# Performance work log

Measured on AMD Instinct MI355X. Metric: run time of the kernel, lower is better.

## Reference

```python
import jax, jax.numpy as jnp
import numpy as np


def setup_inputs() -> dict:
    key = jax.random.key(0)
    k0, k1, k2, k3 = jax.random.split(key, 4)
    B, H, W, C = 2, 128, 128, 512
    N_SPIX = 256  # (H/8)*(W/8) superpixels on an 8-px grid
    x = jax.random.normal(k0, (B, H, W, C), jnp.float32)
    sims = jax.random.uniform(k1, (B, H, W, 9), jnp.float32)
    sinds = jax.random.randint(k2, (B, H, W, 9), 0, N_SPIX, jnp.int32)
    W_qk = jax.random.normal(k3, (C, 2 * C), jnp.float32) * 0.02
    b_qk = jnp.zeros((2 * C,), jnp.float32)
    return {"x": x, "sims": sims, "sinds": sinds, "W_qk": W_qk, "b_qk": b_qk,
            "kernel_size": 7, "num_heads": 4}


def reference(x, sims, sinds, W_qk, b_qk, kernel_size, num_heads):
    """Soft-neighborhood superpixel attention scores.

    attn[b,g,si,h,w,ki] = <q[b,g,h,w], k[b,g,hj,wj]> + log p_j(s)
    where (hj,wj) is the ki-th pixel of the clamped (NATTEN-style) KxK window
    around (h,w), s = sinds[b,h,w,si] is the si-th neighboring-superpixel id
    of pixel (h,w), and p_j(s) = sum_m sims[b,hj,wj,m] * [sinds[b,hj,wj,m]==s]
    (the soft probability that key pixel j belongs to superpixel s; entries
    where s is not among j's 9 neighbor superpixels stay at -inf, matching
    the -inf-initialized attn buffer of the CUDA kernel).
    """
    B, H, W, C = x.shape
    K = kernel_size
    hd = C // num_heads
    r = K // 2

    # qk projection -> (B, heads, H, W, hd) for q and k (permute(3,0,4,1,2,5))
    qk = (x @ W_qk + b_qk).reshape(B, H, W, 2, num_heads, hd)
    q = jnp.moveaxis(qk[:, :, :, 0], 3, 1)  # (B,HD,H,W,hd)
    k = jnp.moveaxis(qk[:, :, :, 1], 3, 1)

    # NATTEN clamped window starts
    hs = jnp.clip(jnp.arange(H) - r, 0, H - K)  # (H,)
    ws = jnp.clip(jnp.arange(W) - r, 0, W - K)  # (W,)
    s_i = sinds  # (B,H,W,9): superpixel ids of pixel i's 9 neighbors

    dots, logps = [], []
    for dh in range(K):
        hj = hs + dh  # (H,)
        for dw in range(K):
            wj = ws + dw  # (W,)
            # gather key/sims/sinds at window offset (dh,dw)
            k_off = k[:, :, hj[:, None], wj[None, :], :]        # (B,HD,H,W,hd)
            dots.append(jnp.einsum('bghwf,bghwf->bghw', q, k_off))
            sind_j = sinds[:, hj[:, None], wj[None, :], :]      # (B,H,W,9)
            sim_j = sims[:, hj[:, None], wj[None, :], :]        # (B,H,W,9)
            # p_j(s_i): match i's si-th superpixel against j's 9 ids
            match = sind_j[:, :, :, None, :] == s_i[:, :, :, :, None]  # (B,H,W,9si,9m)
            pj = jnp.sum(jnp.where(match, sim_j[:, :, :, None, :], 0.0), axis=-1)  # (B,H,W,9)
            logps.append(jnp.where(pj > 0, jnp.log(jnp.maximum(pj, 1e-30)), -jnp.inf))

    dots = jnp.stack(dots, axis=-1)            # (B,HD,H,W,K*K)
    logp = jnp.stack(logps, axis=-1)           # (B,H,W,9,K*K)
    logp = jnp.moveaxis(logp, 3, 1)            # (B,9,H,W,K*K)
    attn = dots[:, :, None] + logp[:, None]    # (B,HD,9,H,W,K*K)
    return attn
```

## Files before the change

### kernel.cpp

```cpp
#include <hip/hip_runtime.h>
#include <hip/hip_bf16.h>
#include <math.h>

#define BATCH 2
#define HH 128
#define WW 128
#define CC 512
#define NH 4
#define HD 128
#define KS 7
#define RR 3
#define KK2 49
#define NSI 9

#define GM (BATCH*HH*WW)
#define GK CC
#define GN (2*CC)

#define NEG_HUGE (-1.0e30f)

typedef __attribute__((ext_vector_type(8))) short bf16x8;
typedef __attribute__((ext_vector_type(4))) float f32x4;

__device__ __forceinline__ float sout(float v) {
    return fminf(fmaxf(v, -3.0e38f), 3.0e38f);
}
__device__ __forceinline__ float bflo(unsigned int u) {
    return __builtin_bit_cast(float, u << 16);
}
__device__ __forceinline__ float bfhi(unsigned int u) {
    return __builtin_bit_cast(float, u & 0xffff0000u);
}
__device__ __forceinline__ unsigned short f2bf(float f) {
    unsigned int u = __builtin_bit_cast(unsigned int, f);
    u += 0x7fffu + ((u >> 16) & 1u);
    return (unsigned short)(u >> 16);
}

__device__ __forceinline__ void gl_lds16(const unsigned short* g, unsigned short* l) {
    __builtin_amdgcn_global_load_lds(
        (const __attribute__((address_space(1))) unsigned int*)g,
        (__attribute__((address_space(3))) unsigned int*)l, 16, 0, 0);
}

__global__ __launch_bounds__(256) void prep(const float* __restrict__ x,
                                            unsigned short* __restrict__ xb,
                                            const float* __restrict__ W,
                                            unsigned short* __restrict__ Wt,
                                            int nxc) {
    int bid = blockIdx.x;
    if (bid < nxc) {
        int t = bid * 256 + threadIdx.x;
        const float4* s = (const float4*)(x + (size_t)t * 8);
        float4 v0 = s[0], v1 = s[1];
        bf16x8 pk;
        pk[0] = (short)f2bf(v0.x); pk[1] = (short)f2bf(v0.y);
        pk[2] = (short)f2bf(v0.z); pk[3] = (short)f2bf(v0.w);
        pk[4] = (short)f2bf(v1.x); pk[5] = (short)f2bf(v1.y);
        pk[6] = (short)f2bf(v1.z); pk[7] = (short)f2bf(v1.w);
        *(bf16x8*)(xb + (size_t)t * 8) = pk;
    } else {
        int t = (bid - nxc) * 256 + threadIdx.x;
        int n = t >> 9, k = t & 511;
        Wt[(size_t)n * GK + k] = f2bf(W[(size_t)k * GN + n]);
    }
}

#define TBM 128
#define TBN 128
#define TBK 64

__global__ __launch_bounds__(256, 3) void qk_gemm_async(
        const unsigned short* __restrict__ xb,
        const unsigned short* __restrict__ Wt,
        const float* __restrict__ bias,
        unsigned short* __restrict__ Cout)
{
    __shared__ unsigned short As[TBM * TBK];
    __shared__ unsigned short Bs[TBN * TBK];

    const int bid = blockIdx.x;
    const int xcd = bid & 7, idx = bid >> 3;
    const int m0 = (xcd * 32 + (idx >> 3)) * TBM;
    const int n0 = (idx & 7) * TBN;

    const int tid = threadIdx.x;
    const int lane = tid & 63;
    const int wid = tid >> 6;
    const int wr = wid >> 1, wc = wid & 1;

    f32x4 acc[4][4];
#pragma unroll
    for (int i = 0; i < 4; ++i)
#pragma unroll
        for (int j = 0; j < 4; ++j) acc[i][j] = (f32x4){0.f, 0.f, 0.f, 0.f};

    const int srow = lane >> 3;
    const int scol = (lane & 7) * 8;

    for (int k0 = 0; k0 < GK; k0 += TBK) {
#pragma unroll
        for (int i = 0; i < 4; ++i) {
            int chunk = wid * 4 + i;
            int row = chunk * 8 + srow;
            gl_lds16(xb + (size_t)(m0 + row) * GK + k0 + scol, &As[chunk * 512]);
            gl_lds16(Wt + (size_t)(n0 + row) * GK + k0 + scol, &Bs[chunk * 512]);
        }
        __syncthreads();

#pragma unroll
        for (int ks = 0; ks < 2; ++ks) {
            const int koff = ks * 32 + (lane >> 4) * 8;
            bf16x8 af[4], bfr[4];
#pragma unroll
            for (int i = 0; i < 4; ++i)
                af[i] = *(const bf16x8*)&As[(wr * 64 + i * 16 + (lane & 15)) * TBK + koff];
#pragma unroll
            for (int j = 0; j < 4; ++j)
                bfr[j] = *(const bf16x8*)&Bs[(wc * 64 + j * 16 + (lane & 15)) * TBK + koff];
#pragma unroll
            for (int i = 0; i < 4; ++i)
#pragma unroll
                for (int j = 0; j < 4; ++j)
                    acc[i][j] = __builtin_amdgcn_mfma_f32_16x16x32_bf16(
                        af[i], bfr[j], acc[i][j], 0, 0, 0);
        }
        __syncthreads();
    }

    const int colbase = n0 + wc * 64;
    float bias4[4];
#pragma unroll
    for (int j = 0; j < 4; ++j) bias4[j] = bias[colbase + j * 16 + (lane & 15)];
#pragma unroll
    for (int i = 0; i < 4; ++i)
#pragma unroll
        for (int j = 0; j < 4; ++j)
#pragma unroll
            for (int r = 0; r < 4; ++r) {
                int row = m0 + wr * 64 + i * 16 + (lane >> 4) * 4 + r;
                int col = colbase + j * 16 + (lane & 15);
                Cout[(size_t)row * GN + col] = f2bf(acc[i][j][r] + bias4[j]);
            }
}

#define LDAB 72

__global__ __launch_bounds__(256) void qk_gemm_conv(
        const float* __restrict__ X,
        const unsigned short* __restrict__ Wt,
        const float* __restrict__ bias,
        unsigned short* __restrict__ Cout)
{
    __shared__ unsigned short As[TBM][LDAB];
    __shared__ unsigned short Bs[TBN][LDAB];

    const int m0 = blockIdx.x * TBM;
    const int n0 = blockIdx.y * TBN;
    const int tid = threadIdx.x;
    const int lane = tid & 63;
    const int wid = tid >> 6;
    const int wr = wid >> 1, wc = wid & 1;

    f32x4 acc[4][4];
#pragma unroll
    for (int i = 0; i < 4; ++i)
#pragma unroll
        for (int j = 0; j < 4; ++j) acc[i][j] = (f32x4){0.f, 0.f, 0.f, 0.f};

    const int srow = tid >> 1;
    const int shalf = (tid & 1) * 32;

    for (int k0 = 0; k0 < GK; k0 += TBK) {
        {
            const float* srcA = X + (size_t)(m0 + srow) * GK + k0 + shalf;
#pragma unroll
            for (int i = 0; i < 4; ++i) {
                float4 v0 = ((const float4*)srcA)[i * 2];
                float4 v1 = ((const float4*)srcA)[i * 2 + 1];
                bf16x8 pk;
                pk[0] = (short)f2bf(v0.x); pk[1] = (short)f2bf(v0.y);
                pk[2] = (short)f2bf(v0.z); pk[3] = (short)f2bf(v0.w);
                pk[4] = (short)f2bf(v1.x); pk[5] = (short)f2bf(v1.y);
                pk[6] = (short)f2bf(v1.z); pk[7] = (short)f2bf(v1.w);
                *(bf16x8*)&As[srow][shalf + i * 8] = pk;
            }
        }
        {
            const unsigned short* srcB = Wt + (size_t)(n0 + srow) * GK + k0 + shalf;
#pragma unroll
            for (int i = 0; i < 4; ++i)
                *(uint4*)&Bs[srow][shalf + i * 8] = ((const uint4*)srcB)[i];
        }
        __syncthreads();

#pragma unroll
        for (int ks = 0; ks < 2; ++ks) {
            const int koff = ks * 32 + (lane >> 4) * 8;
            bf16x8 af[4], bfr[4];
#pragma unroll
            for (int i = 0; i < 4; ++i)
                af[i] = *(const bf16x8*)&As[wr * 64 + i * 16 + (lane & 15)][koff];
#pragma unroll
            for (int j = 0; j < 4; ++j)
                bfr[j] = *(const bf16x8*)&Bs[wc * 64 + j * 16 + (lane & 15)][koff];
#pragma unroll
            for (int i = 0; i < 4; ++i)
#pragma unroll
                for (int j = 0; j < 4; ++j)
                    acc[i][j] = __builtin_amdgcn_mfma_f32_16x16x32_bf16(
                        af[i], bfr[j], acc[i][j], 0, 0, 0);
        }
        __syncthreads();
    }

    const int colbase = n0 + wc * 64;
    float bias4[4];
#pragma unroll
    for (int j = 0; j < 4; ++j) bias4[j] = bias[colbase + j * 16 + (lane & 15)];
#pragma unroll
    for (int i = 0; i < 4; ++i)
#pragma unroll
        for (int j = 0; j < 4; ++j)
#pragma unroll
            for (int r = 0; r < 4; ++r) {
                int row = m0 + wr * 64 + i * 16 + (lane >> 4) * 4 + r;
                int col = colbase + j * 16 + (lane & 15);
                Cout[(size_t)row * GN + col] = f2bf(acc[i][j][r] + bias4[j]);
            }
}

#define HALO 14
#define NKROW 196
#define LQK 136
#define LSS 204
#define NIT 13
#define NITEMS (64*KK2)

__global__ __launch_bounds__(256, 3) void attn_mfma(
        const unsigned short* __restrict__ qk,
        const float* __restrict__ sims,
        const int*   __restrict__ sinds,
        float* __restrict__ out)
{
    __shared__ __align__(16) unsigned char smem[53312];
    unsigned short* Ks = (unsigned short*)smem;
    float* Ss = (float*)smem;

    const int bid = blockIdx.x;
    const int spatial = (bid & 7) * 256 + (bid >> 3);
    const int tw = spatial & 15;
    const int th = (spatial >> 4) & 15;
    const int bg = spatial >> 8;
    const int b = bg >> 2, g = bg & 3;

    const int tid = threadIdx.x;
    const int lane = tid & 63;
    const int wm = tid >> 6;

    const int h0 = th * 8, w0 = tw * 8;
    const int hb = min(max(h0 - RR, 0), HH - KS);
    const int wb = min(max(w0 - RR, 0), WW - KS);

    uint4 kb[NIT];
    int jrow[NIT], ccol[NIT];
#pragma unroll
    for (int p = 0; p < NIT; ++p) {
        int o = tid + p * 256;
        int jj = o >> 4, c = o & 15;
        int jr = min(jj, NKROW - 1);
        int hj = min(hb + jr / HALO, HH - 1);
        int wj = min(wb + jr % HALO, WW - 1);
        kb[p] = *(const uint4*)(qk + ((size_t)((b * HH + hj) * WW + wj)) * GN
                                   + CC + g * HD + c * 8);
        jrow[p] = jr; ccol[p] = c;
    }

    const int pl_q = wm * 16 + (lane & 15);
    const size_t qrow = ((size_t)(b * HH + h0 + (pl_q >> 3)) * WW + w0 + (pl_q & 7)) * GN;
    const int kof8 = (lane >> 4) * 8;
    bf16x8 aq[4];
#pragma unroll
    for (int ks = 0; ks < 4; ++ks)
        aq[ks] = *(const bf16x8*)(qk + qrow + g * HD + ks * 32 + kof8);

#pragma unroll
    for (int p = 0; p < NIT; ++p)
        *(uint4*)&Ks[jrow[p] * LQK + ccol[p] * 8] = kb[p];
    __syncthreads();

    __builtin_amdgcn_s_setprio(1);
    f32x4 svals[NIT];
#pragma unroll
    for (int nt = 0; nt < NIT; ++nt) {
        int rB = min(nt * 16 + (lane & 15), NKROW - 1);
        f32x4 sacc = (f32x4){0.f, 0.f, 0.f, 0.f};
#pragma unroll
        for (int ks = 0; ks < 4; ++ks) {
            bf16x8 bk = *(const bf16x8*)&Ks[rB * LQK + ks * 32 + kof8];
            sacc = __builtin_amdgcn_mfma_f32_16x16x32_bf16(aq[ks], bk, sacc, 0, 0, 0);
        }
        svals[nt] = sacc;
    }
    __builtin_amdgcn_s_setprio(0);
    __syncthreads();

#pragma unroll
    for (int nt = 0; nt < NIT; ++nt)
#pragma unroll
        for (int r = 0; r < 4; ++r) {
            int qr = wm * 16 + (lane >> 4) * 4 + r;
            Ss[qr * LSS + nt * 16 + (lane & 15)] = svals[nt][r];
        }
    __syncthreads();

    const size_t plane = (size_t)HH * WW * KK2;
#pragma unroll
    for (int rr = 0; rr < NIT; ++rr) {
        int it = tid + rr * 256;
        if (it < NITEMS) {
            int pl = it / KK2, ki = it % KK2;
            int h = h0 + (pl >> 3), w = w0 + (pl & 7);
            int dh = ki / KS, dw = ki % KS;
            int hj = min(max(h - RR, 0), HH - KS) + dh;
            int wj = min(max(w - RR, 0), WW - KS) + dw;
            int j = (hj - hb) * HALO + (wj - wb);
            float dot = Ss[pl * LSS + j];
            int pix = (b * HH + h) * WW + w;
            int pj  = (b * HH + hj) * WW + wj;

            int sid[NSI], sjd[NSI]; float sjm[NSI];
            const int*   sip = sinds + (size_t)pix * NSI;
            const int*   sjp = sinds + (size_t)pj * NSI;
            const float* smp = sims + (size_t)pj * NSI;
#pragma unroll
            for (int m = 0; m < NSI; ++m) { sid[m] = sip[m]; sjd[m] = sjp[m]; sjm[m] = smp[m]; }

            size_t inner = (size_t)(h * WW + w) * KK2 + ki;
#pragma unroll
            for (int si = 0; si < NSI; ++si) {
                float p = 0.f;
#pragma unroll
                for (int m = 0; m < NSI; ++m) p += (sjd[m] == sid[si]) ? sjm[m] : 0.f;
                float lp = (p > 0.f) ? __logf(fmaxf(p, 1e-30f)) : NEG_HUGE;
                __builtin_nontemporal_store(sout(dot + lp),
                    &out[((size_t)((b * NH + g) * NSI + si)) * plane + inner]);
            }
        }
    }
}

#define FT 8
#define FH 14
#define FNP (FT*FT)
#define FNJ (FH*FH)
#define FDH 64
#define KPAD 68
#define FNITEM (FNP*KK2)
#define FNR 13

__global__ __launch_bounds__(256) void fused_attn(
        const float* __restrict__ x, const float* __restrict__ sims,
        const int* __restrict__ sinds, const float* __restrict__ Wm,
        const float* __restrict__ bias, float* __restrict__ out)
{
    __shared__ unsigned short kt[FNJ][KPAD];
    __shared__ unsigned short qt[FNP][KPAD];

    const int tw = blockIdx.x, th = blockIdx.y;
    const int b = blockIdx.z >> 2, g = blockIdx.z & 3;
    const int tid = threadIdx.x;
    const int hb = min(max(th * FT - RR, 0), HH - KS);
    const int wb = min(max(tw * FT - RR, 0), WW - KS);

    float dacc[FNR];
#pragma unroll
    for (int r = 0; r < FNR; ++r) dacc[r] = 0.f;

    for (int ph = 0; ph < 2; ++ph) {
        const int kcol0 = CC + g * HD + ph * FDH;
        const int qcol0 = g * HD + ph * FDH;

        for (int o = tid; o < FNJ * FDH; o += 256) {
            int j = o >> 6, dd = o & 63;
            int hj = min(hb + j / FH, HH - 1), wj = min(wb + j % FH, WW - 1);
            const float* xr = x + ((size_t)(b * HH + hj) * WW + wj) * CC;
            int col = kcol0 + dd;
            float acc = bias[col];
            for (int c = 0; c < CC; c += 4) {
                float4 xv = *(const float4*)(xr + c);
                acc += xv.x * Wm[(size_t)c * GN + col]
                     + xv.y * Wm[(size_t)(c + 1) * GN + col]
                     + xv.z * Wm[(size_t)(c + 2) * GN + col]
                     + xv.w * Wm[(size_t)(c + 3) * GN + col];
            }
            kt[j][dd] = f2bf(acc);
        }
        for (int o = tid; o < FNP * FDH; o += 256) {
            int i = o >> 6, dd = o & 63;
            int h = th * FT + (i >> 3), w = tw * FT + (i & 7);
            const float* xr = x + ((size_t)(b * HH + h) * WW + w) * CC;
            int col = qcol0 + dd;
            float acc = bias[col];
            for (int c = 0; c < CC; c += 4) {
                float4 xv = *(const float4*)(xr + c);
                acc += xv.x * Wm[(size_t)c * GN + col]
                     + xv.y * Wm[(size_t)(c + 1) * GN + col]
                     + xv.z * Wm[(size_t)(c + 2) * GN + col]
                     + xv.w * Wm[(size_t)(c + 3) * GN + col];
            }
            qt[i][dd] = f2bf(acc);
        }
        __syncthreads();

#pragma unroll
        for (int r = 0; r < FNR; ++r) {
            int it = tid + r * 256;
            if (it < FNITEM) {
                int pl = it / KK2, ki = it % KK2;
                int h = th * FT + (pl >> 3), w = tw * FT + (pl & 7);
                int dh = ki / KS, dw = ki % KS;
                int hj = min(max(h - RR, 0), HH - KS) + dh;
                int wj = min(max(w - RR, 0), WW - KS) + dw;
                int j = (hj - hb) * FH + (wj - wb);
                const unsigned int* qr = (const unsigned int*)&qt[pl][0];
                const unsigned int* kr = (const unsigned int*)&kt[j][0];
                float a = 0.f;
#pragma unroll 8
                for (int d = 0; d < FDH / 2; ++d) {
                    unsigned int qv = qr[d], kv = kr[d];
                    a += bflo(qv) * bflo(kv) + bfhi(qv) * bfhi(kv);
                }
                dacc[r] += a;
            }
        }
        __syncthreads();
    }

    const size_t plane = (size_t)HH * WW * KK2;
#pragma unroll
    for (int r = 0; r < FNR; ++r) {
        int it = tid + r * 256;
        if (it < FNITEM) {
            int pl = it / KK2, ki = it % KK2;
            int h = th * FT + (pl >> 3), w = tw * FT + (pl & 7);
            int dh = ki / KS, dw = ki % KS;
            int hj = min(max(h - RR, 0), HH - KS) + dh;
            int wj = min(max(w - RR, 0), WW - KS) + dw;
            int pix = (b * HH + h) * WW + w;
            int pj  = (b * HH + hj) * WW + wj;

            int sid[NSI], sjd[NSI]; float sjm[NSI];
            const int*   sip = sinds + (size_t)pix * NSI;
            const int*   sjp = sinds + (size_t)pj * NSI;
            const float* smp = sims + (size_t)pj * NSI;
#pragma unroll
            for (int m = 0; m < NSI; ++m) { sid[m] = sip[m]; sjd[m] = sjp[m]; sjm[m] = smp[m]; }

            const size_t inner = (size_t)(h * WW + w) * KK2 + ki;
#pragma unroll
            for (int si = 0; si < NSI; ++si) {
                float p = 0.f;
#pragma unroll
                for (int m = 0; m < NSI; ++m) p += (sjd[m] == sid[si]) ? sjm[m] : 0.f;
                float lp = (p > 0.f) ? __logf(fmaxf(p, 1e-30f)) : NEG_HUGE;
                out[((size_t)((b * NH + g) * NSI + si)) * plane + inner] =
                    sout(dacc[r] + lp);
            }
        }
    }
}

extern "C" void kernel_launch(void* const* d_in, const int* in_sizes, int n_in,
                              void* d_out, int out_size, void* d_ws, size_t ws_size,
                              hipStream_t stream) {
    const float* x     = (const float*)d_in[0];
    const float* sims  = (const float*)d_in[1];
    const int*   sinds = (const int*)d_in[2];
    const float* W_qk  = (const float*)d_in[3];
    const float* b_qk  = (const float*)d_in[4];
    float* out = (float*)d_out;

    const size_t qk_bytes = (size_t)GM * GN * sizeof(unsigned short);
    const size_t wt_bytes = (size_t)GN * GK * sizeof(unsigned short);
    const size_t xb_bytes = (size_t)GM * GK * sizeof(unsigned short);

    if (ws_size >= qk_bytes + wt_bytes + xb_bytes) {
        unsigned short* qk = (unsigned short*)d_ws;
        unsigned short* Wt = (unsigned short*)((char*)d_ws + qk_bytes);
        unsigned short* xb = (unsigned short*)((char*)d_ws + qk_bytes + wt_bytes);

        prep<<<8192 + 2048, 256, 0, stream>>>(x, xb, W_qk, Wt, 8192);
        qk_gemm_async<<<2048, 256, 0, stream>>>(xb, Wt, b_qk, qk);
        attn_mfma<<<2048, 256, 0, stream>>>(qk, sims, sinds, out);
    } else if (ws_size >= qk_bytes + wt_bytes) {
        unsigned short* qk = (unsigned short*)d_ws;
        unsigned short* Wt = (unsigned short*)((char*)d_ws + qk_bytes);

        prep<<<2048, 256, 0, stream>>>(x, nullptr, W_qk, Wt, 0);
        dim3 ggrid(GM / TBM, GN / TBN);
        qk_gemm_conv<<<ggrid, 256, 0, stream>>>(x, Wt, b_qk, qk);
        attn_mfma<<<2048, 256, 0, stream>>>(qk, sims, sinds, out);
    } else {
        dim3 fgrid(WW / FT, HH / FT, BATCH * NH);
        fused_attn<<<fgrid, 256, 0, stream>>>(x, sims, sinds, W_qk, b_qk, out);
    }
}
```

Measured before the change: 164.5 us.

## Precompute log-superpixel-probabilities once in prep and reuse across heads

Moves the per-(pixel, window offset) log p_j(s) computation out of the attention kernel into the prep kernel, storing the nine values as packed bf16 in workspace. The attention kernel then loads these instead of recomputing them for each of the four heads, removing redundant compare/log work. In exchange it adds a roughly 29 MB intermediate write plus repeated reads, and rounds logp to bf16, which loses precision.

Measured after the change: 164.5 us. About the same (-0.0%).

```diff
diff --git a/kernel.cpp b/kernel.cpp
--- a/kernel.cpp
+++ b/kernel.cpp
@@ -16,6 +16,8 @@
 #define GM (BATCH*HH*WW)
 #define GK CC
 #define GN (2*CC)
+#define NPIX (BATCH*HH*WW)
+#define NITEM_ALL (NPIX*KK2)
 
 #define NEG_HUGE (-1.0e30f)
 
@@ -47,7 +49,11 @@
                                             unsigned short* __restrict__ xb,
                                             const float* __restrict__ W,
                                             unsigned short* __restrict__ Wt,
-                                            int nxc) {
+                                            const float* __restrict__ sims,
+                                            const int* __restrict__ sinds,
+                                            uint4* __restrict__ lpA,
+                                            unsigned short* __restrict__ lpB,
+                                            int nxc, int nwt) {
     int bid = blockIdx.x;
     if (bid < nxc) {
         int t = bid * 256 + threadIdx.x;
@@ -59,10 +65,48 @@
         pk[4] = (short)f2bf(v1.x); pk[5] = (short)f2bf(v1.y);
         pk[6] = (short)f2bf(v1.z); pk[7] = (short)f2bf(v1.w);
         *(bf16x8*)(xb + (size_t)t * 8) = pk;
-    } else {
+    } else if (bid < nxc + nwt) {
         int t = (bid - nxc) * 256 + threadIdx.x;
         int n = t >> 9, k = t & 511;
         Wt[(size_t)n * GK + k] = f2bf(W[(size_t)k * GN + n]);
+    } else {
+        int t = (bid - nxc - nwt) * 256 + threadIdx.x;
+        if (t < NITEM_ALL) {
+            int ki  = t % KK2;
+            int pix = t / KK2;
+            int w   = pix & (WW - 1);
+            int tmp = pix >> 7;
+            int h   = tmp & (HH - 1);
+            int b   = tmp >> 7;
+            int dh = ki / KS, dw = ki % KS;
+            int hj = min(max(h - RR, 0), HH - KS) + dh;
+            int wj = min(max(w - RR, 0), WW - KS) + dw;
+            int pj = (b * HH + hj) * WW + wj;
+
+            int sid[NSI], sjd[NSI]; float sjm[NSI];
+            const int*   sip = sinds + (size_t)pix * NSI;
+            const int*   sjp = sinds + (size_t)pj * NSI;
+            const float* smp = sims + (size_t)pj * NSI;
+#pragma unroll
+            for (int m = 0; m < NSI; ++m) { sid[m] = sip[m]; sjd[m] = sjp[m]; sjm[m] = smp[m]; }
+
+            unsigned short lb[NSI];
+#pragma unroll
+            for (int si = 0; si < NSI; ++si) {
+                float p = 0.f;
+#pragma unroll
+                for (int m = 0; m < NSI; ++m) p += (sjd[m] == sid[si]) ? sjm[m] : 0.f;
+                float lp = (p > 0.f) ? __logf(fmaxf(p, 1e-30f)) : NEG_HUGE;
+                lb[si] = f2bf(lp);
+            }
+            uint4 va;
+            va.x = (unsigned int)lb[0] | ((unsigned int)lb[1] << 16);
+            va.y = (unsigned int)lb[2] | ((unsigned int)lb[3] << 16);
+            va.z = (unsigned int)lb[4] | ((unsigned int)lb[5] << 16);
+            va.w = (unsigned int)lb[6] | ((unsigned int)lb[7] << 16);
+            lpA[t] = va;
+            lpB[t] = lb[8];
+        }
     }
 }
 
@@ -237,7 +281,117 @@
 #define NIT 13
 #define NITEMS (64*KK2)
 
-__global__ __launch_bounds__(256, 3) void attn_mfma(
+__global__ __launch_bounds__(256, 3) void attn_mfma_lp(
+        const unsigned short* __restrict__ qk,
+        const uint4* __restrict__ lpA,
+        const unsigned short* __restrict__ lpB,
+        float* __restrict__ out)
+{
+    __shared__ __align__(16) unsigned char smem[53312];
+    unsigned short* Ks = (unsigned short*)smem;
+    float* Ss = (float*)smem;
+
+    const int bid = blockIdx.x;
+    const int spatial = (bid & 7) * 256 + (bid >> 3);
+    const int tw = spatial & 15;
+    const int th = (spatial >> 4) & 15;
+    const int bg = spatial >> 8;
+    const int b = bg >> 2, g = bg & 3;
+
+    const int tid = threadIdx.x;
+    const int lane = tid & 63;
+    const int wm = tid >> 6;
+
+    const int h0 = th * 8, w0 = tw * 8;
+    const int hb = min(max(h0 - RR, 0), HH - KS);
+    const int wb = min(max(w0 - RR, 0), WW - KS);
+
+    uint4 kb[NIT];
+    int jrow[NIT], ccol[NIT];
+#pragma unroll
+    for (int p = 0; p < NIT; ++p) {
+        int o = tid + p * 256;
+        int jj = o >> 4, c = o & 15;
+        int jr = min(jj, NKROW - 1);
+        int hj = min(hb + jr / HALO, HH - 1);
+        int wj = min(wb + jr % HALO, WW - 1);
+        kb[p] = *(const uint4*)(qk + ((size_t)((b * HH + hj) * WW + wj)) * GN
+                                   + CC + g * HD + c * 8);
+        jrow[p] = jr; ccol[p] = c;
+    }
+
+    const int pl_q = wm * 16 + (lane & 15);
+    const size_t qrow = ((size_t)(b * HH + h0 + (pl_q >> 3)) * WW + w0 + (pl_q & 7)) * GN;
+    const int kof8 = (lane >> 4) * 8;
+    bf16x8 aq[4];
+#pragma unroll
+    for (int ks = 0; ks < 4; ++ks)
+        aq[ks] = *(const bf16x8*)(qk + qrow + g * HD + ks * 32 + kof8);
+
+#pragma unroll
+    for (int p = 0; p < NIT; ++p)
+        *(uint4*)&Ks[jrow[p] * LQK + ccol[p] * 8] = kb[p];
+    __syncthreads();
+
+    __builtin_amdgcn_s_setprio(1);
+    f32x4 svals[NIT];
+#pragma unroll
+    for (int nt = 0; nt < NIT; ++nt) {
+        int rB = min(nt * 16 + (lane & 15), NKROW - 1);
+        f32x4 sacc = (f32x4){0.f, 0.f, 0.f, 0.f};
+#pragma unroll
+        for (int ks = 0; ks < 4; ++ks) {
+            bf16x8 bk = *(const bf16x8*)&Ks[rB * LQK + ks * 32 + kof8];
+            sacc = __builtin_amdgcn_mfma_f32_16x16x32_bf16(aq[ks], bk, sacc, 0, 0, 0);
+        }
+        svals[nt] = sacc;
+    }
+    __builtin_amdgcn_s_setprio(0);
+    __syncthreads();
+
+#pragma unroll
+    for (int nt = 0; nt < NIT; ++nt)
+#pragma unroll
+        for (int r = 0; r < 4; ++r) {
+            int qr = wm * 16 + (lane >> 4) * 4 + r;
+            Ss[qr * LSS + nt * 16 + (lane & 15)] = svals[nt][r];
+        }
+    __syncthreads();
+
+    const size_t plane = (size_t)HH * WW * KK2;
+#pragma unroll
+    for (int rr = 0; rr < NIT; ++rr) {
+        int it = tid + rr * 256;
+        if (it < NITEMS) {
+            int pl = it / KK2, ki = it % KK2;
+            int h = h0 + (pl >> 3), w = w0 + (pl & 7);
+            int dh = ki / KS, dw = ki % KS;
+            int hj = min(max(h - RR, 0), HH - KS) + dh;
+            int wj = min(max(w - RR, 0), WW - KS) + dw;
+            int j = (hj - hb) * HALO + (wj - wb);
+            float dot = Ss[pl * LSS + j];
+            int pix = (b * HH + h) * WW + w;
+            size_t item = (size_t)pix * KK2 + ki;
+
+            uint4 va = lpA[item];
+            unsigned int vb = lpB[item];
+            float lp[NSI];
+            lp[0] = bflo(va.x); lp[1] = bfhi(va.x);
+            lp[2] = bflo(va.y); lp[3] = bfhi(va.y);
+            lp[4] = bflo(va.z); lp[5] = bfhi(va.z);
+            lp[6] = bflo(va.w); lp[7] = bfhi(va.w);
+            lp[8] = bflo(vb);
+
+            size_t inner = (size_t)(h * WW + w) * KK2 + ki;
+#pragma unroll
+            for (int si = 0; si < NSI; ++si)
+                __builtin_nontemporal_store(sout(dot + lp[si]),
+                    &out[((size_t)((b * NH + g) * NSI + si)) * plane + inner]);
+        }
+    }
+}
+
+__global__ __launch_bounds__(256, 3) void attn_mfma_full(
         const unsigned short* __restrict__ qk,
         const float* __restrict__ sims,
         const int*   __restrict__ sinds,
@@ -342,8 +496,8 @@
                 float p = 0.f;
 #pragma unroll
                 for (int m = 0; m < NSI; ++m) p += (sjd[m] == sid[si]) ? sjm[m] : 0.f;
-                float lp = (p > 0.f) ? __logf(fmaxf(p, 1e-30f)) : NEG_HUGE;
-                __builtin_nontemporal_store(sout(dot + lp),
+                float lpv = (p > 0.f) ? __logf(fmaxf(p, 1e-30f)) : NEG_HUGE;
+                __builtin_nontemporal_store(sout(dot + lpv),
                     &out[((size_t)((b * NH + g) * NSI + si)) * plane + inner]);
             }
         }
@@ -484,23 +638,31 @@
     const size_t qk_bytes = (size_t)GM * GN * sizeof(unsigned short);
     const size_t wt_bytes = (size_t)GN * GK * sizeof(unsigned short);
     const size_t xb_bytes = (size_t)GM * GK * sizeof(unsigned short);
-
-    if (ws_size >= qk_bytes + wt_bytes + xb_bytes) {
+    const size_t lpA_bytes = (size_t)NITEM_ALL * sizeof(uint4);
+    const size_t lpB_bytes = (size_t)NITEM_ALL * sizeof(unsigned short);
+
+    if (ws_size >= qk_bytes + wt_bytes + xb_bytes + lpA_bytes + lpB_bytes) {
         unsigned short* qk = (unsigned short*)d_ws;
         unsigned short* Wt = (unsigned short*)((char*)d_ws + qk_bytes);
         unsigned short* xb = (unsigned short*)((char*)d_ws + qk_bytes + wt_bytes);
-
-        prep<<<8192 + 2048, 256, 0, stream>>>(x, xb, W_qk, Wt, 8192);
+        uint4* lpA = (uint4*)((char*)d_ws + qk_bytes + wt_bytes + xb_bytes);
+        unsigned short* lpB = (unsigned short*)((char*)d_ws + qk_bytes + wt_bytes
+                                                + xb_bytes + lpA_bytes);
+
+        const int nxc = 8192, nwt = 2048, nlp = (NITEM_ALL + 255) / 256;
+        prep<<<nxc + nwt + nlp, 256, 0, stream>>>(x, xb, W_qk, Wt,
+                                                  sims, sinds, lpA, lpB, nxc, nwt);
         qk_gemm_async<<<2048, 256, 0, stream>>>(xb, Wt, b_qk, qk);
-        attn_mfma<<<2048, 256, 0, stream>>>(qk, sims, sinds, out);
+        attn_mfma_lp<<<2048, 256, 0, stream>>>(qk, lpA, lpB, out);
     } else if (ws_size >= qk_bytes + wt_bytes) {
         unsigned short* qk = (unsigned short*)d_ws;
         unsigned short* Wt = (unsigned short*)((char*)d_ws + qk_bytes);
 
-        prep<<<2048, 256, 0, stream>>>(x, nullptr, W_qk, Wt, 0);
+        prep<<<2048, 256, 0, stream>>>(x, nullptr, W_qk, Wt,
+                                       nullptr, nullptr, nullptr, nullptr, 0, 2048);
         dim3 ggrid(GM / TBM, GN / TBN);
         qk_gemm_conv<<<ggrid, 256, 0, stream>>>(x, Wt, b_qk, qk);
-        attn_mfma<<<2048, 256, 0, stream>>>(qk, sims, sinds, out);
+        attn_mfma_full<<<2048, 256, 0, stream>>>(qk, sims, sinds, out);
     } else {
         dim3 fgrid(WW / FT, HH / FT, BATCH * NH);
         fused_attn<<<fgrid, 256, 0, stream>>>(x, sims, sinds, W_qk, b_qk, out);
```
